# Kernel optimization log

Measured on AMD Instinct MI355X. Metric: run time of the kernel, lower is better.

Reference implementation:

```python
import jax, jax.numpy as jnp
import numpy as np
from jax import lax

PAD = (2, 1)        # pad=(2,1) from init, applied to both H and W
UPSAMPLE_F = 2      # kernel scaled by upsample_f**2


def make_kernel(k1d, upsample_f):
    k = jnp.asarray(k1d, dtype=jnp.float32)
    k = k[None, :] * k[:, None]          # 1D -> separable 2D outer product
    k = k / jnp.sum(k)                   # normalize to sum 1
    if upsample_f > 1:
        k = k * (upsample_f ** 2)
    return k                             # [4, 4]


def setup_inputs() -> dict:
    key = jax.random.key(0)
    x = jax.random.normal(key, (16, 512, 64, 64), dtype=jnp.float32)
    kernel = make_kernel([1, 3, 3, 1], UPSAMPLE_F)
    return {"x": x, "kernel": kernel}


def reference(x, kernel):
    # upfirdn2d(x, kernel, up=1, down=1, pad=(2,1)):
    # pad H and W by (2,1), then TRUE convolution (kernel flipped) applied
    # depthwise (same FIR kernel on every channel).
    n, c, h, w = x.shape
    kh, kw = kernel.shape
    wflip = jnp.flip(kernel, (0, 1))                     # true conv = flip + correlate
    wdw = jnp.broadcast_to(wflip[None, None], (c, 1, kh, kw))  # [C,1,kh,kw] depthwise
    out = lax.conv_general_dilated(
        x, wdw,
        window_strides=(1, 1),
        padding=(PAD, PAD),
        feature_group_count=c,
        dimension_numbers=("NCHW", "OIHW", "NCHW"),
    )
    return out  # [N, C, H, W] (same spatial size: 64+2+1-4+1 = 64)
```

## Files before the change

kernel.cpp:

```cpp
#include <hip/hip_runtime.h>


#define PW 64
#define PH 64
#define CHUNK 16

__global__ __launch_bounds__(256) void blur_shfl_kernel(
    const float* __restrict__ x, float* __restrict__ out) {
    const int t = threadIdx.x;
    const int lane16 = t & 15;
    const int grp = t >> 4;
    const int y0 = (grp >> 2) * CHUNK;
    const int plane = blockIdx.x * 4 + (grp & 3);

    const float* __restrict__ src = x + (size_t)plane * (PH * PW) + lane16 * 4;
    float* __restrict__ dst = out + (size_t)plane * (PH * PW) + lane16 * 4;

    float4 hA = make_float4(0.f, 0.f, 0.f, 0.f);
    float4 hB = hA, hC = hA;

    #pragma unroll
    for (int i = 0; i < CHUNK + 3; ++i) {
        const int y = y0 - 2 + i;
        float4 v = make_float4(0.f, 0.f, 0.f, 0.f);
        if (y >= 0 && y < PH) {
            v = *reinterpret_cast<const float4*>(src + y * PW);
        }

        float pz = __shfl_up(v.z, 1, 16);
        float pw = __shfl_up(v.w, 1, 16);
        float nx = __shfl_down(v.x, 1, 16);
        if (lane16 == 0)  { pz = 0.f; pw = 0.f; }
        if (lane16 == 15) { nx = 0.f; }
        float4 hD;
        hD.x = 0.75f * (pw  + v.x) + 0.25f * (pz  + v.y);
        hD.y = 0.75f * (v.x + v.y) + 0.25f * (pw  + v.z);
        hD.z = 0.75f * (v.y + v.z) + 0.25f * (v.x + v.w);
        hD.w = 0.75f * (v.z + v.w) + 0.25f * (v.y + nx);

        if (i >= 3) {
            const int yo = y - 1;
            float4 o;
            o.x = 0.25f * (hA.x + hD.x) + 0.75f * (hB.x + hC.x);
            o.y = 0.25f * (hA.y + hD.y) + 0.75f * (hB.y + hC.y);
            o.z = 0.25f * (hA.z + hD.z) + 0.75f * (hB.z + hC.z);
            o.w = 0.25f * (hA.w + hD.w) + 0.75f * (hB.w + hC.w);
            *reinterpret_cast<float4*>(dst + yo * PW) = o;
        }
        hA = hB; hB = hC; hC = hD;
    }
}

extern "C" void kernel_launch(void* const* d_in, const int* in_sizes, int n_in,
                              void* d_out, int out_size, void* d_ws, size_t ws_size,
                              hipStream_t stream) {
    const float* x = (const float*)d_in[0];
    float* out = (float*)d_out;
    const int nplanes = in_sizes[0] / (PH * PW);
    blur_shfl_kernel<<<nplanes / 4, 256, 0, stream>>>(x, out);
}
```

Before: 49.80 us.

## Stage horizontal blur in LDS and do vertical pass from shared memory

Replaces the per-thread rolling vertical window (16-row chunks with 3 halo rows reloaded from global) with a one-plane-per-block design. The block first computes the horizontal FIR into padded LDS, synchronizes, then reads four LDS rows per output for the vertical FIR. This removes redundant halo global loads and gives fully coalesced loads up front with more memory-level parallelism. In exchange it adds about 18KB of LDS per block, a barrier, and four times more blocks.

```diff
diff --git a/kernel.cpp b/kernel.cpp
--- a/kernel.cpp
+++ b/kernel.cpp
@@ -3,51 +3,67 @@
 
 #define PW 64
 #define PH 64
-#define CHUNK 16
+#define LDW 68
+#define ROWS (PH + 3)
 
-__global__ __launch_bounds__(256) void blur_shfl_kernel(
+__global__ __launch_bounds__(256) void blur_fused_kernel(
     const float* __restrict__ x, float* __restrict__ out) {
+    __shared__ float s_h[ROWS * LDW];
+
     const int t = threadIdx.x;
+    const int plane = blockIdx.x;
+    const float* __restrict__ src = x + (size_t)plane * (PH * PW);
+    float* __restrict__ dst = out + (size_t)plane * (PH * PW);
+
+    {
+        const float4 z = make_float4(0.f, 0.f, 0.f, 0.f);
+        if (t < 34)
+            reinterpret_cast<float4*>(&s_h[0])[t] = z;
+        else if (t < 51)
+            reinterpret_cast<float4*>(&s_h[(ROWS - 1) * LDW])[t - 34] = z;
+    }
+
     const int lane16 = t & 15;
-    const int grp = t >> 4;
-    const int y0 = (grp >> 2) * CHUNK;
-    const int plane = blockIdx.x * 4 + (grp & 3);
-
-    const float* __restrict__ src = x + (size_t)plane * (PH * PW) + lane16 * 4;
-    float* __restrict__ dst = out + (size_t)plane * (PH * PW) + lane16 * 4;
-
-    float4 hA = make_float4(0.f, 0.f, 0.f, 0.f);
-    float4 hB = hA, hC = hA;
 
     #pragma unroll
-    for (int i = 0; i < CHUNK + 3; ++i) {
-        const int y = y0 - 2 + i;
-        float4 v = make_float4(0.f, 0.f, 0.f, 0.f);
-        if (y >= 0 && y < PH) {
-            v = *reinterpret_cast<const float4*>(src + y * PW);
-        }
+    for (int k = 0; k < 4; ++k) {
+        const int f = t + k * 256;
+        const int y = f >> 4;
+        const int x0 = (f & 15) << 2;
+        const float4 v = reinterpret_cast<const float4*>(src)[f];
 
         float pz = __shfl_up(v.z, 1, 16);
         float pw = __shfl_up(v.w, 1, 16);
         float nx = __shfl_down(v.x, 1, 16);
         if (lane16 == 0)  { pz = 0.f; pw = 0.f; }
         if (lane16 == 15) { nx = 0.f; }
-        float4 hD;
-        hD.x = 0.75f * (pw  + v.x) + 0.25f * (pz  + v.y);
-        hD.y = 0.75f * (v.x + v.y) + 0.25f * (pw  + v.z);
-        hD.z = 0.75f * (v.y + v.z) + 0.25f * (v.x + v.w);
-        hD.w = 0.75f * (v.z + v.w) + 0.25f * (v.y + nx);
 
-        if (i >= 3) {
-            const int yo = y - 1;
-            float4 o;
-            o.x = 0.25f * (hA.x + hD.x) + 0.75f * (hB.x + hC.x);
-            o.y = 0.25f * (hA.y + hD.y) + 0.75f * (hB.y + hC.y);
-            o.z = 0.25f * (hA.z + hD.z) + 0.75f * (hB.z + hC.z);
-            o.w = 0.25f * (hA.w + hD.w) + 0.75f * (hB.w + hC.w);
-            *reinterpret_cast<float4*>(dst + yo * PW) = o;
-        }
-        hA = hB; hB = hC; hC = hD;
+        float4 h;
+        h.x = 0.75f * (pw  + v.x) + 0.25f * (pz  + v.y);
+        h.y = 0.75f * (v.x + v.y) + 0.25f * (pw  + v.z);
+        h.z = 0.75f * (v.y + v.z) + 0.25f * (v.x + v.w);
+        h.w = 0.75f * (v.z + v.w) + 0.25f * (v.y + nx);
+
+        *reinterpret_cast<float4*>(&s_h[(y + 2) * LDW + x0]) = h;
+    }
+    __syncthreads();
+
+    #pragma unroll
+    for (int k = 0; k < 4; ++k) {
+        const int f = t + k * 256;
+        const int y = f >> 4;
+        const int x0 = (f & 15) << 2;
+        const float* __restrict__ b = &s_h[y * LDW + x0];
+        const float4 hA = *reinterpret_cast<const float4*>(b);
+        const float4 hB = *reinterpret_cast<const float4*>(b + LDW);
+        const float4 hC = *reinterpret_cast<const float4*>(b + 2 * LDW);
+        const float4 hD = *reinterpret_cast<const float4*>(b + 3 * LDW);
+        float4 o;
+        o.x = 0.25f * (hA.x + hD.x) + 0.75f * (hB.x + hC.x);
+        o.y = 0.25f * (hA.y + hD.y) + 0.75f * (hB.y + hC.y);
+        o.z = 0.25f * (hA.z + hD.z) + 0.75f * (hB.z + hC.z);
+        o.w = 0.25f * (hA.w + hD.w) + 0.75f * (hB.w + hC.w);
+        reinterpret_cast<float4*>(dst)[f] = o;
     }
 }
 
@@ -57,5 +73,5 @@
     const float* x = (const float*)d_in[0];
     float* out = (float*)d_out;
     const int nplanes = in_sizes[0] / (PH * PW);
-    blur_shfl_kernel<<<nplanes / 4, 256, 0, stream>>>(x, out);
+    blur_fused_kernel<<<nplanes, 256, 0, stream>>>(x, out);
 }
```

New measurement: 44.08 us. 1.13x faster.
